# Performance work log

Measured on AMD Instinct MI355X. Metric: run time of the kernel, lower is better.

The kernel has to match this reference:

```python
import jax, jax.numpy as jnp
import numpy as np

B, S, DIM = 1, 1024, 1024
H, G = 16, 4
HPG = H // G
DK = 64
DV = 64
L_CMP, D_STR = 32, 16      # compression block length l, stride d
L_SEL, N_SEL = 64, 8       # selection block length, num selected blocks
W_WIN = 512                # sliding window
TAU = 1.0
GATE_H = 32
SCALE = 1.0 / float(np.sqrt(DK))
S_CMP = (S - L_CMP) // D_STR + 1          # number of compressed blocks
N_BLK = (S + L_SEL - 1) // L_SEL          # number of selection blocks

# static Eq.9 mapping: fractional overlap of compressed block c with selection block m
_c0 = np.arange(S_CMP) * D_STR
_m0 = np.arange(N_BLK) * L_SEL
_ov = np.maximum(0, np.minimum(_c0[:, None] + L_CMP, _m0[None, :] + L_SEL)
                 - np.maximum(_c0[:, None], _m0[None, :]))
M_MAP = jnp.asarray(_ov.astype(np.float32) / float(L_CMP))   # [S_CMP, N_BLK]

_POOL_IDX = np.arange(S_CMP)[:, None] * D_STR + np.arange(L_CMP)[None, :]  # [S_CMP, L_CMP]


def _rope(x, pos):
    # llama-style rotary embedding; pos broadcasts against x's leading dims
    half = x.shape[-1] // 2
    inv = 1.0 / (10000.0 ** (jnp.arange(half, dtype=jnp.float32) / half))
    ang = pos[..., None] * inv
    cos, sin = jnp.cos(ang), jnp.sin(ang)
    x1, x2 = x[..., :half], x[..., half:]
    return jnp.concatenate([x1 * cos - x2 * sin, x1 * sin + x2 * cos], axis=-1)


def _masked_softmax(scores, mask):
    p = jax.nn.softmax(jnp.where(mask, scores, -1e30), axis=-1)
    return jnp.where(mask.any(axis=-1, keepdims=True), p, 0.0)


def _forward(x, wq, wk_sel, wv_sel, wk_win, wv_win, wk_cmp, wv_cmp, w_out,
             g1_w, g1_b, g2_w, g2_b):
    pos = jnp.arange(S, dtype=jnp.float32)
    t = jnp.arange(S)
    q = _rope((x @ wq.T).reshape(B, S, G, HPG, DK), pos[None, :, None, None])  # [B,S,G,h,Dk]

    def k_proj(w):
        k = jnp.transpose((x @ w.T).reshape(B, S, G, DK), (0, 2, 1, 3))  # [B,G,S,Dk]
        return _rope(k, pos[None, None, :])

    def v_proj(w):
        return jnp.transpose((x @ w.T).reshape(B, S, G, DV), (0, 2, 1, 3))  # [B,G,S,Dv]

    # --- compressed branch (phi = avg pooling over blocks of l with stride d) ---
    k_cmp = k_proj(wk_cmp); v_cmp = v_proj(wv_cmp)
    Kc = k_cmp[:, :, _POOL_IDX, :].mean(axis=3)  # [B,G,S_CMP,Dk]
    Vc = v_cmp[:, :, _POOL_IDX, :].mean(axis=3)  # [B,G,S_CMP,Dv]
    sc_cmp = jnp.einsum('bsghd,bgcd->bsghc', q, Kc) * SCALE
    cmp_mask = (jnp.arange(S_CMP) * D_STR + (L_CMP - 1))[None, :] <= t[:, None]  # [S,S_CMP]
    p_cmp = _masked_softmax(sc_cmp, cmp_mask[None, :, None, None, :])
    O_cmp = jnp.einsum('bsghc,bgcd->bsghd', p_cmp, Vc)

    # --- selection branch: map compressed scores to selection blocks (Eq.9),
    #     group-sum over heads, force block 0 + current block, top-k, gather ---
    p_slc = jnp.einsum('bsghc,cm->bsgm', p_cmp, M_MAP)  # sums over heads h -> [B,S,G,N_BLK]
    blk = jnp.arange(N_BLK)
    forced = (blk[None, :] == 0) | (blk[None, :] == (t // L_SEL)[:, None])  # [S,N_BLK]
    causal = (blk[None, :] * L_SEL) <= t[:, None]                            # [S,N_BLK]
    sel_logits = jnp.where(causal[None, :, None, :],
                           p_slc + 1e6 * forced[None, :, None, :], -1e9)
    _, top_idx = jax.lax.top_k(sel_logits, N_SEL)  # [B,S,G,N_SEL]
    tok = (top_idx[..., None] * L_SEL + jnp.arange(L_SEL)).reshape(B, S, G, N_SEL * L_SEL)
    tok_g = jnp.transpose(tok, (0, 2, 1, 3))  # [B,G,S,L]
    k_sel = k_proj(wk_sel); v_sel = v_proj(wv_sel)
    bi = jnp.arange(B)[:, None, None, None]
    gi = jnp.arange(G)[None, :, None, None]
    Kg = k_sel[bi, gi, tok_g]  # [B,G,S,L,Dk]
    Vg = v_sel[bi, gi, tok_g]  # [B,G,S,L,Dv]
    sc_sel = jnp.einsum('bsghd,bgsld->bsghl', q, Kg) * SCALE
    tok_mask = (tok <= t[None, :, None, None])[:, :, :, None, :]  # causal within gathered tokens
    p_sel = _masked_softmax(sc_sel, tok_mask)
    O_sel = jnp.einsum('bsghl,bgsld->bsghd', p_sel, Vg)

    # --- sliding window branch ---
    k_win = k_proj(wk_win); v_win = v_proj(wv_win)
    sc_win = jnp.einsum('bsghd,bgtd->bsght', q, k_win) * SCALE
    wmask = (t[None, :] <= t[:, None]) & (t[None, :] > t[:, None] - W_WIN)  # [S,S]
    p_win = _masked_softmax(sc_win, wmask[None, :, None, None, :])
    O_win = jnp.einsum('bsght,bgtd->bsghd', p_win, v_win)

    # --- gate MLP on group-pooled q ---
    qg = q.mean(axis=3)                              # [B,S,G,Dk]
    h1 = jax.nn.silu(qg @ g1_w.T + g1_b)
    glog = (h1 @ g2_w.T + g2_b) / max(TAU, 1e-6)
    pg = jax.nn.softmax(glog, axis=-1)               # [B,S,G,3]
    top2 = jax.lax.top_k(glog, 2)[0]
    peaked = jax.lax.stop_gradient((top2[..., 0] - top2[..., 1]) > 50.0)
    onehot = jax.nn.one_hot(jnp.argmax(glog, axis=-1), 3, dtype=pg.dtype)
    pg = jnp.where(peaked[..., None], onehot, pg)

    O = (pg[..., 0][..., None, None] * O_cmp
         + pg[..., 1][..., None, None] * O_sel
         + pg[..., 2][..., None, None] * O_win)      # [B,S,G,h,Dv]
    return O.reshape(B, S, H * DV) @ w_out.T


def setup_inputs() -> dict:
    key = jax.random.key(0)
    ks = jax.random.split(key, 11)
    n = lambda k, shp, s=0.02: jax.random.normal(k, shp, dtype=jnp.float32) * s
    return {
        'x': jax.random.normal(ks[0], (B, S, DIM), dtype=jnp.float32),
        'wq': n(ks[1], (H * DK, DIM)),
        'wk_sel': n(ks[2], (G * DK, DIM)),
        'wv_sel': n(ks[3], (G * DV, DIM)),
        'wk_win': n(ks[4], (G * DK, DIM)),
        'wv_win': n(ks[5], (G * DV, DIM)),
        'wk_cmp': n(ks[6], (G * DK, DIM)),
        'wv_cmp': n(ks[7], (G * DV, DIM)),
        'w_out': n(ks[8], (DIM, H * DV)),
        'g1_w': n(ks[9], (GATE_H, DK), 0.1),
        'g1_b': jnp.zeros((GATE_H,), jnp.float32),
        'g2_w': n(ks[10], (3, GATE_H), 0.05),  # xavier gain 0.1 -> small init
        'g2_b': jnp.zeros((3,), jnp.float32),
    }


def reference(x, wq, wk_sel, wv_sel, wk_win, wv_win, wk_cmp, wv_cmp, w_out,
              g1_w, g1_b, g2_w, g2_b):
    return _forward(x, wq, wk_sel, wv_sel, wk_win, wv_win, wk_cmp, wv_cmp, w_out,
                    g1_w, g1_b, g2_w, g2_b)
```

## Files before the change

kernel.cpp:

```cpp
#include <hip/hip_runtime.h>
#include <math.h>

#define SLEN   1024
#define NGRP   4
#define NHEAD  16
#define HPGRP  4
#define DKV    64
#define SCMP   63
#define NBLK   16
#define NSELK  8
#define WWIN   512
#define SCALEF 0.125f
#define QBLK   16
#define EXPOFF 8.0f
#define CSTR   2560

typedef __attribute__((ext_vector_type(4))) float f32x4;
typedef __attribute__((ext_vector_type(8))) short bf16x8;

__device__ __forceinline__ unsigned short f2bf(float f) {
  unsigned u = __float_as_uint(f);
  u += 0x7FFFu + ((u >> 16) & 1u);
  return (unsigned short)(u >> 16);
}
__device__ __forceinline__ unsigned pack2(float a, float b) {
  return (unsigned)f2bf(a) | ((unsigned)f2bf(b) << 16);
}
__device__ __forceinline__ bf16x8 pack8(float4 a, float4 b) {
  union { bf16x8 v; unsigned u[4]; } u;
  u.u[0] = pack2(a.x, a.y); u.u[1] = pack2(a.z, a.w);
  u.u[2] = pack2(b.x, b.y); u.u[3] = pack2(b.z, b.w);
  return u.v;
}

struct ConvJobs {
  const float* src[9];
  unsigned* dst[9];
  int n4[9];
  int cnt;
};

__global__ __launch_bounds__(256) void conv_f32_bf16(ConvJobs jb) {
  const int stride = gridDim.x * blockDim.x;
  for (int t = 0; t < jb.cnt; ++t) {
    const float4* s = (const float4*)jb.src[t];
    uint2* d = (uint2*)jb.dst[t];
    const int n4 = jb.n4[t];
    for (int i = blockIdx.x * blockDim.x + threadIdx.x; i < n4; i += stride) {
      const float4 v = s[i];
      uint2 o;
      o.x = pack2(v.x, v.y);
      o.y = pack2(v.z, v.w);
      d[i] = o;
    }
  }
}

__global__ __launch_bounds__(256) void conv_add_bf16(
    const float* __restrict__ a, const float* __restrict__ b, uint2* __restrict__ d)
{
  const int i = blockIdx.x * 256 + threadIdx.x;
  const float4 va = ((const float4*)a)[i];
  const float4 vb = ((const float4*)b)[i];
  uint2 o;
  o.x = pack2(va.x + vb.x, va.y + vb.y);
  o.y = pack2(va.z + vb.z, va.w + vb.w);
  d[i] = o;
}

__device__ __forceinline__ void gload_lds16(const unsigned short* g, unsigned short* l) {
  __builtin_amdgcn_global_load_lds(
      (const __attribute__((address_space(1))) void*)g,
      (__attribute__((address_space(3))) void*)l, 16, 0, 0);
}

__device__ __forceinline__ void gemm_mfma_body(
    const unsigned short* __restrict__ A, const unsigned short* __restrict__ W,
    float* __restrict__ C, int N, int K, int bm, int bn, int tid)
{
  __shared__ unsigned short As[3][2048];
  __shared__ unsigned short Bs[3][2048];
  const int lane = tid & 63;
  const int wave = tid >> 6;
  const int wr = wave >> 1, wc = wave & 1;

  const int sub = tid >> 6;
  const int kh  = (tid >> 4) & 3;
  const int row = tid & 15;
  const unsigned short* aSrc = A + (size_t)(bm + sub * 16 + row) * K + kh * 8;
  const unsigned short* bSrc = W + (size_t)(bn + sub * 16 + row) * K + kh * 8;
  const int slot = tid * 8;

  f32x4 acc[2][2];
#pragma unroll
  for (int m = 0; m < 2; ++m)
#pragma unroll
    for (int n = 0; n < 2; ++n) acc[m][n] = (f32x4){0.f, 0.f, 0.f, 0.f};

  const int NIT = K >> 5;
  gload_lds16(aSrc + 0,  &As[0][slot]);
  gload_lds16(bSrc + 0,  &Bs[0][slot]);
  gload_lds16(aSrc + 32, &As[1][slot]);
  gload_lds16(bSrc + 32, &Bs[1][slot]);

  for (int i = 0; i < NIT; ++i) {
    __builtin_amdgcn_sched_barrier(0);
    if (i + 1 < NIT) asm volatile("s_waitcnt vmcnt(2)" ::: "memory");
    else             asm volatile("s_waitcnt vmcnt(0)" ::: "memory");
    __builtin_amdgcn_s_barrier();
    __builtin_amdgcn_sched_barrier(0);
    if (i + 2 < NIT) {
      const int nb = (i + 2) % 3;
      gload_lds16(aSrc + (i + 2) * 32, &As[nb][slot]);
      gload_lds16(bSrc + (i + 2) * 32, &Bs[nb][slot]);
    }
    const int cur = i % 3;
    const bf16x8 a0 = *(const bf16x8*)(&As[cur][(wr * 2 + 0) * 512 + lane * 8]);
    const bf16x8 a1 = *(const bf16x8*)(&As[cur][(wr * 2 + 1) * 512 + lane * 8]);
    const bf16x8 b0 = *(const bf16x8*)(&Bs[cur][(wc * 2 + 0) * 512 + lane * 8]);
    const bf16x8 b1 = *(const bf16x8*)(&Bs[cur][(wc * 2 + 1) * 512 + lane * 8]);
    acc[0][0] = __builtin_amdgcn_mfma_f32_16x16x32_bf16(a0, b0, acc[0][0], 0, 0, 0);
    acc[0][1] = __builtin_amdgcn_mfma_f32_16x16x32_bf16(a0, b1, acc[0][1], 0, 0, 0);
    acc[1][0] = __builtin_amdgcn_mfma_f32_16x16x32_bf16(a1, b0, acc[1][0], 0, 0, 0);
    acc[1][1] = __builtin_amdgcn_mfma_f32_16x16x32_bf16(a1, b1, acc[1][1], 0, 0, 0);
  }

  const int cr = (lane >> 4) * 4;
  const int cc = lane & 15;
#pragma unroll
  for (int m = 0; m < 2; ++m)
#pragma unroll
    for (int n = 0; n < 2; ++n) {
      float* cp = C + (size_t)(bm + wr * 32 + m * 16 + cr) * N + (bn + wc * 32 + n * 16 + cc);
#pragma unroll
      for (int r = 0; r < 4; ++r) cp[(size_t)r * N] = acc[m][n][r];
    }
}

__global__ __launch_bounds__(256) void gemm_bf16(
    const unsigned short* __restrict__ A, const unsigned short* __restrict__ W,
    float* __restrict__ C, int N, int K)
{
  gemm_mfma_body(A, W, C, N, K, blockIdx.y * 64, blockIdx.x * 64, threadIdx.x);
}

__global__ __launch_bounds__(256) void mid_kernel(
    const float* __restrict__ C,
    const float* __restrict__ g1w, const float* __restrict__ g1b,
    const float* __restrict__ g2w, const float* __restrict__ g2b,
    unsigned short* __restrict__ q_b,
    unsigned short* __restrict__ kselb, unsigned short* __restrict__ kwinb,
    float* __restrict__ gates,
    unsigned short* __restrict__ vselT, unsigned short* __restrict__ vwinT,
    unsigned short* __restrict__ KcB, unsigned short* __restrict__ VcTB)
{
  const int b = blockIdx.x;
  const int t = threadIdx.x;

  __shared__ float csS[32], snS[32];
  __shared__ float qs[1024];
  __shared__ float qgS[4][64];
  __shared__ float h1S[4][32];
  __shared__ float glS[4][3];
  __shared__ float tile[32][33];
  __shared__ float csP[32][32], snP[32][32];

  if (b < 1024) {
    const int s = b;
    if (t < 32) {
      const float inv = powf(10000.f, -(float)t * (1.f / 32.f));
      float sn, cs;
      sincosf((float)s * inv, &sn, &cs);
      csS[t] = cs; snS[t] = sn;
    }
    __syncthreads();
    {
      const int ht = t >> 4;
      const float* qr = C + (size_t)s * CSTR + ht * 64;
#pragma unroll
      for (int i = 0; i < 2; ++i) {
        const int dd = (t & 15) * 2 + i;
        const float x1 = qr[dd], x2 = qr[dd + 32];
        qs[ht * 64 + dd]      = x1 * csS[dd] - x2 * snS[dd];
        qs[ht * 64 + dd + 32] = x1 * snS[dd] + x2 * csS[dd];
      }
    }
    {
      const int which = t >> 7;
      const int g = (t >> 5) & 3, dd = t & 31;
      const float* src = C + (size_t)s * CSTR + (which ? 1536 : 1024) + g * 64;
      unsigned short* dst = (which ? kwinb : kselb) + (size_t)s * 256 + g * 64;
      const float x1 = src[dd], x2 = src[dd + 32];
      dst[dd]      = f2bf(x1 * csS[dd] - x2 * snS[dd]);
      dst[dd + 32] = f2bf(x1 * snS[dd] + x2 * csS[dd]);
    }
    __syncthreads();
    {
      uint2 o;
      o.x = pack2(qs[t * 4 + 0], qs[t * 4 + 1]);
      o.y = pack2(qs[t * 4 + 2], qs[t * 4 + 3]);
      *(uint2*)(q_b + (size_t)s * 1024 + t * 4) = o;
    }
    {
      const int g = t >> 6, d = t & 63;
      qgS[g][d] = (qs[g * 256 + d] + qs[g * 256 + 64 + d] +
                   qs[g * 256 + 128 + d] + qs[g * 256 + 192 + d]) * 0.25f;
    }
    __syncthreads();
    if (t < 128) {
      const int g = t >> 5, j = t & 31;
      float a = g1b[j];
      for (int d = 0; d < 64; ++d) a += qgS[g][d] * g1w[j * 64 + d];
      h1S[g][j] = a / (1.f + expf(-a));
    }
    __syncthreads();
    if (t < 16) {
      const int g = t >> 2, rr = t & 3;
      if (rr < 3) {
        float a = g2b[rr];
        for (int j = 0; j < 32; ++j) a += h1S[g][j] * g2w[rr * 32 + j];
        glS[g][rr] = a;
      }
    }
    __syncthreads();
    if (t < 4) {
      const int g = t;
      const float gl0 = glS[g][0], gl1 = glS[g][1], gl2 = glS[g][2];
      const float m1 = fmaxf(gl0, fmaxf(gl1, gl2));
      const float e0 = expf(gl0 - m1), e1 = expf(gl1 - m1), e2 = expf(gl2 - m1);
      const float inv = 1.f / (e0 + e1 + e2);
      float p0 = e0 * inv, p1 = e1 * inv, p2 = e2 * inv;
      int am = 0; float best = gl0;
      if (gl1 > best) { best = gl1; am = 1; }
      if (gl2 > best) { best = gl2; am = 2; }
      float second = -INFINITY;
      if (am != 0) second = fmaxf(second, gl0);
      if (am != 1) second = fmaxf(second, gl1);
      if (am != 2) second = fmaxf(second, gl2);
      if (best - second > 50.f) {
        p0 = (am == 0) ? 1.f : 0.f; p1 = (am == 1) ? 1.f : 0.f; p2 = (am == 2) ? 1.f : 0.f;
      }
      float* o = gates + (size_t)(s * 4 + g) * 3;
      o[0] = p0; o[1] = p1; o[2] = p2;
    }
  } else if (b < 1536) {
    const int idx = b - 1024;
    const int tr = (idx & 31) * 32, tc = ((idx >> 5) & 7) * 32;
    const int z = idx >> 8;
    const int off = z ? 1792 : 1280;
    unsigned short* dst = z ? vwinT : vselT;
    const int r = t >> 5, c = t & 31;
#pragma unroll
    for (int i = 0; i < 4; ++i)
      tile[r + i * 8][c] = C[(size_t)(tr + r + i * 8) * CSTR + off + tc + c];
    __syncthreads();
#pragma unroll
    for (int i = 0; i < 4; ++i)
      dst[(size_t)(tc + r + i * 8) * 1024 + tr + c] = f2bf(tile[c][r + i * 8]);
  } else {
    const int c = b - 1536;
    const int g = t >> 6, d = t & 63;
#pragma unroll
    for (int qq = 0; qq < 4; ++qq) {
      const int idx = t * 4 + qq;
      const int j = idx >> 5, dd = idx & 31;
      const float inv = powf(10000.f, -(float)dd * (1.f / 32.f));
      float sn, cs;
      sincosf((float)(c * 16 + j) * inv, &sn, &cs);
      csP[j][dd] = cs; snP[j][dd] = sn;
    }
    __syncthreads();
    float ak = 0.f, av = 0.f;
    if (c < SCMP) {
      const int d2 = d & 31;
      for (int j = 0; j < 32; ++j) {
        const int pos = c * 16 + j;
        const float k1 = C[(size_t)pos * CSTR + 2048 + g * 64 + d2];
        const float k2 = C[(size_t)pos * CSTR + 2048 + g * 64 + d2 + 32];
        ak += (d < 32) ? (k1 * csP[j][d2] - k2 * snP[j][d2])
                       : (k1 * snP[j][d2] + k2 * csP[j][d2]);
        av += C[(size_t)pos * CSTR + 2304 + g * 64 + d];
      }
      ak *= (1.f / 32.f); av *= (1.f / 32.f);
    }
    KcB[(size_t)(g * 64 + c) * 64 + d] = f2bf(ak);
    VcTB[(size_t)(g * 64 + d) * 64 + c] = f2bf(av);
  }
}

__device__ __forceinline__ void stage_tile(
    const unsigned short* kbase, int krow,
    const unsigned short* vbase, int vrow,
    unsigned short* Kb, unsigned short* Vb, int tid)
{
#pragma unroll
  for (int i = 0; i < 2; ++i) {
    const int t2 = tid + i * 256;
    const int sf = t2 >> 7, sks = (t2 >> 6) & 1, skh = (t2 >> 4) & 3, stk = t2 & 15;
    gload_lds16(kbase + (size_t)(16 * sf + stk) * krow + sks * 32 + skh * 8, Kb + t2 * 8);
    gload_lds16(vbase + (size_t)(16 * sf + stk) * vrow + sks * 32 + skh * 8, Vb + t2 * 8);
  }
}

template<int BR>
__device__ __forceinline__ void attn_compute(
    int b, int s0, int l,
    bf16x8 aq0, bf16x8 aq1,
    float (&ps)[4], f32x4 (&Oa)[4],
    const unsigned short* Klds, const unsigned short* Vlds,
    float (*Pw)[68], const unsigned* selmaskS)
{
  const int kg = l >> 4, lr = l & 15;
  f32x4 sc[4];
  __builtin_amdgcn_s_setprio(1);
#pragma unroll
  for (int f = 0; f < 4; ++f) {
    sc[f] = (f32x4){0.f, 0.f, 0.f, 0.f};
    sc[f] = __builtin_amdgcn_mfma_f32_16x16x32_bf16(
        aq0, *(const bf16x8*)(Klds + (f * 2 + 0) * 512 + l * 8), sc[f], 0, 0, 0);
    sc[f] = __builtin_amdgcn_mfma_f32_16x16x32_bf16(
        aq1, *(const bf16x8*)(Klds + (f * 2 + 1) * 512 + l * 8), sc[f], 0, 0, 0);
  }
  __builtin_amdgcn_s_setprio(0);

#pragma unroll
  for (int r = 0; r < 4; ++r) {
    const int lrow = kg * 4 + r;
    const int sr = s0 + lrow;
#pragma unroll
    for (int f = 0; f < 4; ++f) {
      const int tok = b * 64 + 16 * f + lr;
      bool ok;
      if (BR == 0)      ok = (tok < SCMP) && (tok * 16 + 31 <= sr);
      else if (BR == 1) ok = ((selmaskS[lrow] >> b) & 1u) && (tok <= sr);
      else              ok = (tok <= sr) && (tok > sr - WWIN);
      const float p = ok ? __expf(sc[f][r] * SCALEF - EXPOFF) : 0.f;
      Pw[lrow][16 * f + lr] = p;
      ps[r] += p;
    }
  }
  asm volatile("s_waitcnt lgkmcnt(0)" ::: "memory");
#pragma unroll
  for (int ks = 0; ks < 2; ++ks) {
    const float4 pa0 = *(const float4*)&Pw[lr][ks * 32 + kg * 8];
    const float4 pa1 = *(const float4*)&Pw[lr][ks * 32 + kg * 8 + 4];
    const bf16x8 pa = pack8(pa0, pa1);
    __builtin_amdgcn_s_setprio(1);
#pragma unroll
    for (int f = 0; f < 4; ++f)
      Oa[f] = __builtin_amdgcn_mfma_f32_16x16x32_bf16(
          pa, *(const bf16x8*)(Vlds + (f * 2 + ks) * 512 + l * 8), Oa[f], 0, 0, 0);
    __builtin_amdgcn_s_setprio(0);
  }
}

#define TILE_SYNC(more) do { \
    __builtin_amdgcn_sched_barrier(0); \
    if (more) asm volatile("s_waitcnt vmcnt(4)" ::: "memory"); \
    else      asm volatile("s_waitcnt vmcnt(0)" ::: "memory"); \
    __builtin_amdgcn_sched_barrier(0); \
    __builtin_amdgcn_s_barrier(); \
    __builtin_amdgcn_sched_barrier(0); \
  } while (0)

__global__ __launch_bounds__(256) void attn_mfma_kernel(
    const unsigned short* __restrict__ qb,
    const unsigned short* __restrict__ kselb,
    const unsigned short* __restrict__ vselT,
    const unsigned short* __restrict__ kwinb,
    const unsigned short* __restrict__ vwinT,
    const unsigned short* __restrict__ KcB,
    const unsigned short* __restrict__ VcTB,
    const float* __restrict__ gates,
    float* __restrict__ Ocs, float* __restrict__ Owin)
{
  const int qt = blockIdx.x;
  const int g  = blockIdx.y;
  const int z  = blockIdx.z;
  const int s0 = qt * QBLK;
  const int tid = threadIdx.x;
  const int w = tid >> 6, l = tid & 63;
  const int kg = l >> 4, lr = l & 15;
  const int bmax = s0 >> 6;

  __shared__ unsigned short Klds[3][4096];
  __shared__ unsigned short Vlds[3][4096];
  __shared__ float Plds[4][16][68];
  __shared__ float lgS[QBLK][16];
  __shared__ float lcS[4][16];
  __shared__ unsigned selmaskS[QBLK];
  __shared__ int selListS[16];
  __shared__ int nselS;

  if (tid < QBLK) selmaskS[tid] = 0u;

  const int sq = s0 + lr;
  const unsigned short* qrow = qb + (size_t)(sq * 16 + g * 4 + w) * 64;
  const bf16x8 aq0 = *(const bf16x8*)(qrow + kg * 8);
  const bf16x8 aq1 = *(const bf16x8*)(qrow + 32 + kg * 8);

  float gv[3][4];
#pragma unroll
  for (int r = 0; r < 4; ++r) {
    const int sr = s0 + kg * 4 + r;
    const float* gp = gates + (size_t)(sr * 4 + g) * 3;
    gv[0][r] = gp[0]; gv[1][r] = gp[1]; gv[2][r] = gp[2];
  }

  f32x4 Ot[4];
#pragma unroll
  for (int f = 0; f < 4; ++f) Ot[f] = (f32x4){0.f, 0.f, 0.f, 0.f};

  float ps[4], ls[4];
  f32x4 Oa[4];

#define ARESET() do { \
    _Pragma("unroll") for (int r = 0; r < 4; ++r) ps[r] = 0.f; \
    _Pragma("unroll") for (int f = 0; f < 4; ++f) Oa[f] = (f32x4){0.f,0.f,0.f,0.f}; \
  } while (0)
#define REDUCE_LS() do { \
    _Pragma("unroll") for (int r = 0; r < 4; ++r) { \
      ls[r] = ps[r]; \
      ls[r] += __shfl_xor(ls[r], 1); ls[r] += __shfl_xor(ls[r], 2); \
      ls[r] += __shfl_xor(ls[r], 4); ls[r] += __shfl_xor(ls[r], 8); } \
  } while (0)
#define AFINAL(bi) do { \
    _Pragma("unroll") for (int f = 0; f < 4; ++f) \
    _Pragma("unroll") for (int r = 0; r < 4; ++r) \
      Ot[f][r] += gv[bi][r] * ((ls[r] > 0.f) ? (Oa[f][r] / ls[r]) : 0.f); \
  } while (0)

  if (z == 0) {
    ARESET();
    stage_tile(KcB + (size_t)g * 64 * 64, 64, VcTB + (size_t)g * 64 * 64, 64,
               Klds[0], Vlds[0], tid);
    TILE_SYNC(0);
    attn_compute<0>(0, s0, l, aq0, aq1, ps, Oa, Klds[0], Vlds[0], Plds[w], selmaskS);
    REDUCE_LS();
    if ((l & 15) == 0) {
#pragma unroll
      for (int r = 0; r < 4; ++r) lcS[w][kg * 4 + r] = ls[r];
    }
    AFINAL(0);
    __syncthreads();

    {
      const int row = tid >> 4, mm = tid & 15;
      float psl = 0.f;
#pragma unroll
      for (int hh = 0; hh < 4; ++hh) {
        const float lc = lcS[hh][row];
        if (lc > 0.f) {
          const int cb = 4 * mm;
          float a = Plds[hh][row][cb] + Plds[hh][row][cb + 1] + Plds[hh][row][cb + 2];
          if (cb >= 1)       a += 0.5f * Plds[hh][row][cb - 1];
          if (cb + 3 < SCMP) a += 0.5f * Plds[hh][row][cb + 3];
          psl += a / lc;
        }
      }
      const bool causal = (mm <= bmax);
      const bool forced = (mm == 0) || (mm == bmax);
      lgS[row][mm] = causal ? (psl + (forced ? 1e6f : 0.f)) : -1e9f;
    }
    __syncthreads();
    {
      const int row = tid >> 4, mm = tid & 15;
      const float my = lgS[row][mm];
      int rank = 0;
#pragma unroll
      for (int m2 = 0; m2 < 16; ++m2) {
        const float v = lgS[row][m2];
        if (v > my || (v == my && m2 < mm)) ++rank;
      }
      if (rank < NSELK && mm <= bmax) atomicOr(&selmaskS[row], 1u << mm);
    }
    __syncthreads();
    if (tid == 0) {
      unsigned u = 0;
      for (int r = 0; r < QBLK; ++r) u |= selmaskS[r];
      int n = 0;
      for (int b = 0; b < 16; ++b) if ((u >> b) & 1u) selListS[n++] = b;
      nselS = n;
    }
    __syncthreads();
    const int nt = nselS;

    ARESET();
    {
      const int b0 = selListS[0];
      stage_tile(kselb + (size_t)b0 * 64 * 256 + g * 64, 256,
                 vselT + (size_t)g * 64 * 1024 + b0 * 64, 1024,
                 Klds[0], Vlds[0], tid);
      for (int i = 0; i < nt; ++i) {
        if (i + 1 < nt) {
          const int bn = selListS[i + 1];
          const int nb = (i + 1) % 3;
          stage_tile(kselb + (size_t)bn * 64 * 256 + g * 64, 256,
                     vselT + (size_t)g * 64 * 1024 + bn * 64, 1024,
                     Klds[nb], Vlds[nb], tid);
        }
        TILE_SYNC(i + 1 < nt);
        attn_compute<1>(selListS[i], s0, l, aq0, aq1, ps, Oa,
                        Klds[i % 3], Vlds[i % 3], Plds[w], selmaskS);
        __builtin_amdgcn_sched_barrier(0);
      }
    }
    REDUCE_LS();
    AFINAL(1);

#pragma unroll
    for (int f = 0; f < 4; ++f)
#pragma unroll
      for (int r = 0; r < 4; ++r) {
        const int sr = s0 + kg * 4 + r;
        Ocs[(size_t)(sr * 16 + g * 4 + w) * 64 + 16 * f + lr] = Ot[f][r];
      }
  } else {
    ARESET();
    const int blo = (s0 >= (WWIN - 1)) ? ((s0 - (WWIN - 1)) >> 6) : 0;
    const int nt = bmax - blo + 1;
    stage_tile(kwinb + (size_t)blo * 64 * 256 + g * 64, 256,
               vwinT + (size_t)g * 64 * 1024 + blo * 64, 1024,
               Klds[0], Vlds[0], tid);
    for (int i = 0; i < nt; ++i) {
      if (i + 1 < nt) {
        const int bn = blo + i + 1;
        const int nb = (i + 1) % 3;
        stage_tile(kwinb + (size_t)bn * 64 * 256 + g * 64, 256,
                   vwinT + (size_t)g * 64 * 1024 + bn * 64, 1024,
                   Klds[nb], Vlds[nb], tid);
      }
      TILE_SYNC(i + 1 < nt);
      attn_compute<2>(blo + i, s0, l, aq0, aq1, ps, Oa,
                      Klds[i % 3], Vlds[i % 3], Plds[w], selmaskS);
      __builtin_amdgcn_sched_barrier(0);
    }
    REDUCE_LS();
    AFINAL(2);

#pragma unroll
    for (int f = 0; f < 4; ++f)
#pragma unroll
      for (int r = 0; r < 4; ++r) {
        const int sr = s0 + kg * 4 + r;
        Owin[(size_t)(sr * 16 + g * 4 + w) * 64 + 16 * f + lr] = Ot[f][r];
      }
  }
#undef ARESET
#undef REDUCE_LS
#undef AFINAL
}

extern "C" void kernel_launch(void* const* d_in, const int* in_sizes, int n_in,
                              void* d_out, int out_size, void* d_ws, size_t ws_size,
                              hipStream_t stream) {
  const float* x      = (const float*)d_in[0];
  const float* wq     = (const float*)d_in[1];
  const float* wk_sel = (const float*)d_in[2];
  const float* wv_sel = (const float*)d_in[3];
  const float* wk_win = (const float*)d_in[4];
  const float* wv_win = (const float*)d_in[5];
  const float* wk_cmp = (const float*)d_in[6];
  const float* wv_cmp = (const float*)d_in[7];
  const float* w_out  = (const float*)d_in[8];
  const float* g1w    = (const float*)d_in[9];
  const float* g1b    = (const float*)d_in[10];
  const float* g2w    = (const float*)d_in[11];
  const float* g2b    = (const float*)d_in[12];

  float* ws = (float*)d_ws;
  float* Cq    = ws;
  float* gts   = Cq + 2621440;
  float* Ocs   = gts + 12288;
  float* Owin  = Ocs + 1048576;

  unsigned short* xb     = (unsigned short*)(Owin + 1048576);
  unsigned short* wqkvb  = xb + 1048576;
  unsigned short* w_outb = wqkvb + 2621440;
  unsigned short* q_b    = w_outb + 1048576;
  unsigned short* kselb  = q_b + 1048576;
  unsigned short* kwinb  = kselb + 262144;
  unsigned short* vselT  = kwinb + 262144;
  unsigned short* vwinT  = vselT + 262144;
  unsigned short* KcB    = vwinT + 262144;
  unsigned short* VcTB   = KcB + 16384;

  ConvJobs j1 = {};
  j1.cnt = 9;
  j1.src[0] = x;      j1.dst[0] = (unsigned*)xb;                        j1.n4[0] = 262144;
  j1.src[1] = wq;     j1.dst[1] = (unsigned*)wqkvb;                     j1.n4[1] = 262144;
  j1.src[2] = wk_sel; j1.dst[2] = (unsigned*)(wqkvb + 1048576);         j1.n4[2] = 65536;
  j1.src[3] = wv_sel; j1.dst[3] = (unsigned*)(wqkvb + 1048576+262144);  j1.n4[3] = 65536;
  j1.src[4] = wk_win; j1.dst[4] = (unsigned*)(wqkvb + 1048576+524288);  j1.n4[4] = 65536;
  j1.src[5] = wv_win; j1.dst[5] = (unsigned*)(wqkvb + 1048576+786432);  j1.n4[5] = 65536;
  j1.src[6] = wk_cmp; j1.dst[6] = (unsigned*)(wqkvb + 1048576+1048576); j1.n4[6] = 65536;
  j1.src[7] = wv_cmp; j1.dst[7] = (unsigned*)(wqkvb + 1048576+1310720); j1.n4[7] = 65536;
  j1.src[8] = w_out;  j1.dst[8] = (unsigned*)w_outb;                    j1.n4[8] = 262144;
  conv_f32_bf16<<<1024, 256, 0, stream>>>(j1);

  gemm_bf16<<<dim3(40, 16), 256, 0, stream>>>(xb, wqkvb, Cq, CSTR, 1024);

  mid_kernel<<<1600, 256, 0, stream>>>(Cq, g1w, g1b, g2w, g2b,
                                       q_b, kselb, kwinb, gts,
                                       vselT, vwinT, KcB, VcTB);

  attn_mfma_kernel<<<dim3(64, 4, 2), 256, 0, stream>>>(
      q_b, kselb, vselT, kwinb, vwinT, KcB, VcTB, gts, Ocs, Owin);

  conv_add_bf16<<<1024, 256, 0, stream>>>(Ocs, Owin, (uint2*)xb);
  gemm_bf16<<<dim3(16, 16), 256, 0, stream>>>(xb, w_outb, (float*)d_out, 1024, 1024);
}
```

Before: 112.7 us.

## Split attention into compressed pass and split-K selected/window tile kernel with combine

The fused attention kernel is split into three kernels. The first computes the compressed branch and top-k block selection and writes the selection masks to global memory. The second processes selected and window tiles with work split in two per branch, giving four z-slices instead of two, and writes unnormalised numerators and row sums. A combine kernel then normalises, gates, sums and converts the result to bf16. Probabilities are also stored to LDS as bf16 rather than fp32. The aim is to balance load across blocks and raise parallelism, at the cost of an extra launch and roughly 16 MB of partial-result traffic.

After: 115.1 us. 2.1% more time.

```diff
diff --git a/kernel.cpp b/kernel.cpp
--- a/kernel.cpp
+++ b/kernel.cpp
@@ -54,18 +54,6 @@
       d[i] = o;
     }
   }
-}
-
-__global__ __launch_bounds__(256) void conv_add_bf16(
-    const float* __restrict__ a, const float* __restrict__ b, uint2* __restrict__ d)
-{
-  const int i = blockIdx.x * 256 + threadIdx.x;
-  const float4 va = ((const float4*)a)[i];
-  const float4 vb = ((const float4*)b)[i];
-  uint2 o;
-  o.x = pack2(va.x + vb.x, va.y + vb.y);
-  o.y = pack2(va.z + vb.z, va.w + vb.w);
-  d[i] = o;
 }
 
 __device__ __forceinline__ void gload_lds16(const unsigned short* g, unsigned short* l) {
@@ -302,58 +290,6 @@
   }
 }
 
-template<int BR>
-__device__ __forceinline__ void attn_compute(
-    int b, int s0, int l,
-    bf16x8 aq0, bf16x8 aq1,
-    float (&ps)[4], f32x4 (&Oa)[4],
-    const unsigned short* Klds, const unsigned short* Vlds,
-    float (*Pw)[68], const unsigned* selmaskS)
-{
-  const int kg = l >> 4, lr = l & 15;
-  f32x4 sc[4];
-  __builtin_amdgcn_s_setprio(1);
-#pragma unroll
-  for (int f = 0; f < 4; ++f) {
-    sc[f] = (f32x4){0.f, 0.f, 0.f, 0.f};
-    sc[f] = __builtin_amdgcn_mfma_f32_16x16x32_bf16(
-        aq0, *(const bf16x8*)(Klds + (f * 2 + 0) * 512 + l * 8), sc[f], 0, 0, 0);
-    sc[f] = __builtin_amdgcn_mfma_f32_16x16x32_bf16(
-        aq1, *(const bf16x8*)(Klds + (f * 2 + 1) * 512 + l * 8), sc[f], 0, 0, 0);
-  }
-  __builtin_amdgcn_s_setprio(0);
-
-#pragma unroll
-  for (int r = 0; r < 4; ++r) {
-    const int lrow = kg * 4 + r;
-    const int sr = s0 + lrow;
-#pragma unroll
-    for (int f = 0; f < 4; ++f) {
-      const int tok = b * 64 + 16 * f + lr;
-      bool ok;
-      if (BR == 0)      ok = (tok < SCMP) && (tok * 16 + 31 <= sr);
-      else if (BR == 1) ok = ((selmaskS[lrow] >> b) & 1u) && (tok <= sr);
-      else              ok = (tok <= sr) && (tok > sr - WWIN);
-      const float p = ok ? __expf(sc[f][r] * SCALEF - EXPOFF) : 0.f;
-      Pw[lrow][16 * f + lr] = p;
-      ps[r] += p;
-    }
-  }
-  asm volatile("s_waitcnt lgkmcnt(0)" ::: "memory");
-#pragma unroll
-  for (int ks = 0; ks < 2; ++ks) {
-    const float4 pa0 = *(const float4*)&Pw[lr][ks * 32 + kg * 8];
-    const float4 pa1 = *(const float4*)&Pw[lr][ks * 32 + kg * 8 + 4];
-    const bf16x8 pa = pack8(pa0, pa1);
-    __builtin_amdgcn_s_setprio(1);
-#pragma unroll
-    for (int f = 0; f < 4; ++f)
-      Oa[f] = __builtin_amdgcn_mfma_f32_16x16x32_bf16(
-          pa, *(const bf16x8*)(Vlds + (f * 2 + ks) * 512 + l * 8), Oa[f], 0, 0, 0);
-    __builtin_amdgcn_s_setprio(0);
-  }
-}
-
 #define TILE_SYNC(more) do { \
     __builtin_amdgcn_sched_barrier(0); \
     if (more) asm volatile("s_waitcnt vmcnt(4)" ::: "memory"); \
@@ -363,16 +299,199 @@
     __builtin_amdgcn_sched_barrier(0); \
   } while (0)
 
-__global__ __launch_bounds__(256) void attn_mfma_kernel(
+__global__ __launch_bounds__(256) void attn_cmp_kernel(
+    const unsigned short* __restrict__ qb,
+    const unsigned short* __restrict__ KcB,
+    const unsigned short* __restrict__ VcTB,
+    const float* __restrict__ gates,
+    float* __restrict__ Ocs, unsigned* __restrict__ selmaskG)
+{
+  const int qt = blockIdx.x;
+  const int g  = blockIdx.y;
+  const int s0 = qt * QBLK;
+  const int tid = threadIdx.x;
+  const int w = tid >> 6, l = tid & 63;
+  const int kg = l >> 4, lr = l & 15;
+  const int bmax = s0 >> 6;
+
+  __shared__ unsigned short Klds[4096];
+  __shared__ unsigned short Vlds[4096];
+  __shared__ float Plds[4][16][68];
+  __shared__ float lgS[QBLK][16];
+  __shared__ float lcS[4][16];
+  __shared__ unsigned selmaskS[QBLK];
+
+  if (tid < QBLK) selmaskS[tid] = 0u;
+
+  const int sq = s0 + lr;
+  const unsigned short* qrow = qb + (size_t)(sq * 16 + g * 4 + w) * 64;
+  const bf16x8 aq0 = *(const bf16x8*)(qrow + kg * 8);
+  const bf16x8 aq1 = *(const bf16x8*)(qrow + 32 + kg * 8);
+
+  float gv0[4];
+#pragma unroll
+  for (int r = 0; r < 4; ++r)
+    gv0[r] = gates[(size_t)((s0 + kg * 4 + r) * 4 + g) * 3];
+
+  float ps[4], ls[4];
+  f32x4 Oa[4];
+#pragma unroll
+  for (int r = 0; r < 4; ++r) ps[r] = 0.f;
+#pragma unroll
+  for (int f = 0; f < 4; ++f) Oa[f] = (f32x4){0.f, 0.f, 0.f, 0.f};
+
+  stage_tile(KcB + (size_t)g * 64 * 64, 64, VcTB + (size_t)g * 64 * 64, 64,
+             Klds, Vlds, tid);
+  TILE_SYNC(0);
+
+  f32x4 sc[4];
+  __builtin_amdgcn_s_setprio(1);
+#pragma unroll
+  for (int f = 0; f < 4; ++f) {
+    sc[f] = (f32x4){0.f, 0.f, 0.f, 0.f};
+    sc[f] = __builtin_amdgcn_mfma_f32_16x16x32_bf16(
+        aq0, *(const bf16x8*)(Klds + (f * 2 + 0) * 512 + l * 8), sc[f], 0, 0, 0);
+    sc[f] = __builtin_amdgcn_mfma_f32_16x16x32_bf16(
+        aq1, *(const bf16x8*)(Klds + (f * 2 + 1) * 512 + l * 8), sc[f], 0, 0, 0);
+  }
+  __builtin_amdgcn_s_setprio(0);
+#pragma unroll
+  for (int r = 0; r < 4; ++r) {
+    const int sr = s0 + kg * 4 + r;
+#pragma unroll
+    for (int f = 0; f < 4; ++f) {
+      const int tok = 16 * f + lr;
+      const bool ok = (tok < SCMP) && (tok * 16 + 31 <= sr);
+      const float p = ok ? __expf(sc[f][r] * SCALEF - EXPOFF) : 0.f;
+      Plds[w][kg * 4 + r][16 * f + lr] = p;
+      ps[r] += p;
+    }
+  }
+  asm volatile("s_waitcnt lgkmcnt(0)" ::: "memory");
+#pragma unroll
+  for (int ks = 0; ks < 2; ++ks) {
+    const float4 pa0 = *(const float4*)&Plds[w][lr][ks * 32 + kg * 8];
+    const float4 pa1 = *(const float4*)&Plds[w][lr][ks * 32 + kg * 8 + 4];
+    const bf16x8 pa = pack8(pa0, pa1);
+    __builtin_amdgcn_s_setprio(1);
+#pragma unroll
+    for (int f = 0; f < 4; ++f)
+      Oa[f] = __builtin_amdgcn_mfma_f32_16x16x32_bf16(
+          pa, *(const bf16x8*)(Vlds + (f * 2 + ks) * 512 + l * 8), Oa[f], 0, 0, 0);
+    __builtin_amdgcn_s_setprio(0);
+  }
+
+#pragma unroll
+  for (int r = 0; r < 4; ++r) {
+    ls[r] = ps[r];
+    ls[r] += __shfl_xor(ls[r], 1); ls[r] += __shfl_xor(ls[r], 2);
+    ls[r] += __shfl_xor(ls[r], 4); ls[r] += __shfl_xor(ls[r], 8);
+  }
+  if ((l & 15) == 0) {
+#pragma unroll
+    for (int r = 0; r < 4; ++r) lcS[w][kg * 4 + r] = ls[r];
+  }
+#pragma unroll
+  for (int f = 0; f < 4; ++f)
+#pragma unroll
+    for (int r = 0; r < 4; ++r) {
+      const int sr = s0 + kg * 4 + r;
+      Ocs[(size_t)(sr * 16 + g * 4 + w) * 64 + 16 * f + lr] =
+          gv0[r] * ((ls[r] > 0.f) ? (Oa[f][r] / ls[r]) : 0.f);
+    }
+  __syncthreads();
+
+  {
+    const int row = tid >> 4, mm = tid & 15;
+    float psl = 0.f;
+#pragma unroll
+    for (int hh = 0; hh < 4; ++hh) {
+      const float lc = lcS[hh][row];
+      if (lc > 0.f) {
+        const int cb = 4 * mm;
+        float a = Plds[hh][row][cb] + Plds[hh][row][cb + 1] + Plds[hh][row][cb + 2];
+        if (cb >= 1)       a += 0.5f * Plds[hh][row][cb - 1];
+        if (cb + 3 < SCMP) a += 0.5f * Plds[hh][row][cb + 3];
+        psl += a / lc;
+      }
+    }
+    const bool causal = (mm <= bmax);
+    const bool forced = (mm == 0) || (mm == bmax);
+    lgS[row][mm] = causal ? (psl + (forced ? 1e6f : 0.f)) : -1e9f;
+  }
+  __syncthreads();
+  {
+    const int row = tid >> 4, mm = tid & 15;
+    const float my = lgS[row][mm];
+    int rank = 0;
+#pragma unroll
+    for (int m2 = 0; m2 < 16; ++m2) {
+      const float v = lgS[row][m2];
+      if (v > my || (v == my && m2 < mm)) ++rank;
+    }
+    if (rank < NSELK && mm <= bmax) atomicOr(&selmaskS[row], 1u << mm);
+  }
+  __syncthreads();
+  if (tid < QBLK) selmaskG[(s0 + tid) * 4 + g] = selmaskS[tid];
+}
+
+template<int BR>
+__device__ __forceinline__ void attn_computeB(
+    int b, int s0, int l,
+    bf16x8 aq0, bf16x8 aq1,
+    float (&ps)[4], f32x4 (&Oa)[4],
+    const unsigned short* Klds, const unsigned short* Vlds,
+    unsigned short (*PwB)[72], const unsigned* selmaskS)
+{
+  const int kg = l >> 4, lr = l & 15;
+  f32x4 sc[4];
+  __builtin_amdgcn_s_setprio(1);
+#pragma unroll
+  for (int f = 0; f < 4; ++f) {
+    sc[f] = (f32x4){0.f, 0.f, 0.f, 0.f};
+    sc[f] = __builtin_amdgcn_mfma_f32_16x16x32_bf16(
+        aq0, *(const bf16x8*)(Klds + (f * 2 + 0) * 512 + l * 8), sc[f], 0, 0, 0);
+    sc[f] = __builtin_amdgcn_mfma_f32_16x16x32_bf16(
+        aq1, *(const bf16x8*)(Klds + (f * 2 + 1) * 512 + l * 8), sc[f], 0, 0, 0);
+  }
+  __builtin_amdgcn_s_setprio(0);
+
+#pragma unroll
+  for (int r = 0; r < 4; ++r) {
+    const int lrow = kg * 4 + r;
+    const int sr = s0 + lrow;
+#pragma unroll
+    for (int f = 0; f < 4; ++f) {
+      const int tok = b * 64 + 16 * f + lr;
+      bool ok;
+      if (BR == 1) ok = ((selmaskS[lrow] >> b) & 1u) && (tok <= sr);
+      else         ok = (tok <= sr) && (tok > sr - WWIN);
+      const float p = ok ? __expf(sc[f][r] * SCALEF - EXPOFF) : 0.f;
+      PwB[lrow][16 * f + lr] = f2bf(p);
+      ps[r] += p;
+    }
+  }
+  asm volatile("s_waitcnt lgkmcnt(0)" ::: "memory");
+#pragma unroll
+  for (int ks = 0; ks < 2; ++ks) {
+    const bf16x8 pa = *(const bf16x8*)&PwB[lr][ks * 32 + kg * 8];
+    __builtin_amdgcn_s_setprio(1);
+#pragma unroll
+    for (int f = 0; f < 4; ++f)
+      Oa[f] = __builtin_amdgcn_mfma_f32_16x16x32_bf16(
+          pa, *(const bf16x8*)(Vlds + (f * 2 + ks) * 512 + l * 8), Oa[f], 0, 0, 0);
+    __builtin_amdgcn_s_setprio(0);
+  }
+}
+
+__global__ __launch_bounds__(256) void attn_tiles_kernel(
     const unsigned short* __restrict__ qb,
     const unsigned short* __restrict__ kselb,
     const unsigned short* __restrict__ vselT,
     const unsigned short* __restrict__ kwinb,
     const unsigned short* __restrict__ vwinT,
-    const unsigned short* __restrict__ KcB,
-    const unsigned short* __restrict__ VcTB,
-    const float* __restrict__ gates,
-    float* __restrict__ Ocs, float* __restrict__ Owin)
+    const unsigned* __restrict__ selmaskG,
+    float* __restrict__ Pnum, float* __restrict__ Pls)
 {
   const int qt = blockIdx.x;
   const int g  = blockIdx.y;
@@ -382,173 +501,130 @@
   const int w = tid >> 6, l = tid & 63;
   const int kg = l >> 4, lr = l & 15;
   const int bmax = s0 >> 6;
+  const bool isSel = (z < 2);
 
   __shared__ unsigned short Klds[3][4096];
   __shared__ unsigned short Vlds[3][4096];
-  __shared__ float Plds[4][16][68];
-  __shared__ float lgS[QBLK][16];
-  __shared__ float lcS[4][16];
+  __shared__ unsigned short PldsB[4][16][72];
   __shared__ unsigned selmaskS[QBLK];
-  __shared__ int selListS[16];
-  __shared__ int nselS;
-
-  if (tid < QBLK) selmaskS[tid] = 0u;
+  __shared__ int listS[16];
+  __shared__ int ntS;
+
+  if (tid < QBLK)
+    selmaskS[tid] = isSel ? selmaskG[(s0 + tid) * 4 + g] : 0u;
+  __syncthreads();
+  if (tid == 0) {
+    int n = 0;
+    if (isSel) {
+      unsigned u = 0;
+      for (int r = 0; r < QBLK; ++r) u |= selmaskS[r];
+      int idx = 0;
+      for (int b = 0; b < 16; ++b)
+        if ((u >> b) & 1u) { if ((idx & 1) == z) listS[n++] = b; ++idx; }
+    } else {
+      const int blo = (s0 >= (WWIN - 1)) ? ((s0 - (WWIN - 1)) >> 6) : 0;
+      for (int b = blo + (z - 2); b <= bmax; b += 2) listS[n++] = b;
+    }
+    ntS = n;
+  }
+  __syncthreads();
+  const int nt = ntS;
 
   const int sq = s0 + lr;
   const unsigned short* qrow = qb + (size_t)(sq * 16 + g * 4 + w) * 64;
   const bf16x8 aq0 = *(const bf16x8*)(qrow + kg * 8);
   const bf16x8 aq1 = *(const bf16x8*)(qrow + 32 + kg * 8);
 
-  float gv[3][4];
-#pragma unroll
-  for (int r = 0; r < 4; ++r) {
-    const int sr = s0 + kg * 4 + r;
-    const float* gp = gates + (size_t)(sr * 4 + g) * 3;
-    gv[0][r] = gp[0]; gv[1][r] = gp[1]; gv[2][r] = gp[2];
-  }
-
-  f32x4 Ot[4];
-#pragma unroll
-  for (int f = 0; f < 4; ++f) Ot[f] = (f32x4){0.f, 0.f, 0.f, 0.f};
+  const unsigned short* kb = isSel ? kselb : kwinb;
+  const unsigned short* vb = isSel ? vselT : vwinT;
 
   float ps[4], ls[4];
   f32x4 Oa[4];
-
-#define ARESET() do { \
-    _Pragma("unroll") for (int r = 0; r < 4; ++r) ps[r] = 0.f; \
-    _Pragma("unroll") for (int f = 0; f < 4; ++f) Oa[f] = (f32x4){0.f,0.f,0.f,0.f}; \
-  } while (0)
-#define REDUCE_LS() do { \
-    _Pragma("unroll") for (int r = 0; r < 4; ++r) { \
-      ls[r] = ps[r]; \
-      ls[r] += __shfl_xor(ls[r], 1); ls[r] += __shfl_xor(ls[r], 2); \
-      ls[r] += __shfl_xor(ls[r], 4); ls[r] += __shfl_xor(ls[r], 8); } \
-  } while (0)
-#define AFINAL(bi) do { \
-    _Pragma("unroll") for (int f = 0; f < 4; ++f) \
-    _Pragma("unroll") for (int r = 0; r < 4; ++r) \
-      Ot[f][r] += gv[bi][r] * ((ls[r] > 0.f) ? (Oa[f][r] / ls[r]) : 0.f); \
-  } while (0)
-
-  if (z == 0) {
-    ARESET();
-    stage_tile(KcB + (size_t)g * 64 * 64, 64, VcTB + (size_t)g * 64 * 64, 64,
-               Klds[0], Vlds[0], tid);
-    TILE_SYNC(0);
-    attn_compute<0>(0, s0, l, aq0, aq1, ps, Oa, Klds[0], Vlds[0], Plds[w], selmaskS);
-    REDUCE_LS();
-    if ((l & 15) == 0) {
-#pragma unroll
-      for (int r = 0; r < 4; ++r) lcS[w][kg * 4 + r] = ls[r];
-    }
-    AFINAL(0);
-    __syncthreads();
-
-    {
-      const int row = tid >> 4, mm = tid & 15;
-      float psl = 0.f;
-#pragma unroll
-      for (int hh = 0; hh < 4; ++hh) {
-        const float lc = lcS[hh][row];
-        if (lc > 0.f) {
-          const int cb = 4 * mm;
-          float a = Plds[hh][row][cb] + Plds[hh][row][cb + 1] + Plds[hh][row][cb + 2];
-          if (cb >= 1)       a += 0.5f * Plds[hh][row][cb - 1];
-          if (cb + 3 < SCMP) a += 0.5f * Plds[hh][row][cb + 3];
-          psl += a / lc;
-        }
-      }
-      const bool causal = (mm <= bmax);
-      const bool forced = (mm == 0) || (mm == bmax);
-      lgS[row][mm] = causal ? (psl + (forced ? 1e6f : 0.f)) : -1e9f;
-    }
-    __syncthreads();
-    {
-      const int row = tid >> 4, mm = tid & 15;
-      const float my = lgS[row][mm];
-      int rank = 0;
-#pragma unroll
-      for (int m2 = 0; m2 < 16; ++m2) {
-        const float v = lgS[row][m2];
-        if (v > my || (v == my && m2 < mm)) ++rank;
-      }
-      if (rank < NSELK && mm <= bmax) atomicOr(&selmaskS[row], 1u << mm);
-    }
-    __syncthreads();
-    if (tid == 0) {
-      unsigned u = 0;
-      for (int r = 0; r < QBLK; ++r) u |= selmaskS[r];
-      int n = 0;
-      for (int b = 0; b < 16; ++b) if ((u >> b) & 1u) selListS[n++] = b;
-      nselS = n;
-    }
-    __syncthreads();
-    const int nt = nselS;
-
-    ARESET();
-    {
-      const int b0 = selListS[0];
-      stage_tile(kselb + (size_t)b0 * 64 * 256 + g * 64, 256,
-                 vselT + (size_t)g * 64 * 1024 + b0 * 64, 1024,
-                 Klds[0], Vlds[0], tid);
-      for (int i = 0; i < nt; ++i) {
-        if (i + 1 < nt) {
-          const int bn = selListS[i + 1];
-          const int nb = (i + 1) % 3;
-          stage_tile(kselb + (size_t)bn * 64 * 256 + g * 64, 256,
-                     vselT + (size_t)g * 64 * 1024 + bn * 64, 1024,
-                     Klds[nb], Vlds[nb], tid);
-        }
-        TILE_SYNC(i + 1 < nt);
-        attn_compute<1>(selListS[i], s0, l, aq0, aq1, ps, Oa,
-                        Klds[i % 3], Vlds[i % 3], Plds[w], selmaskS);
-        __builtin_amdgcn_sched_barrier(0);
-      }
-    }
-    REDUCE_LS();
-    AFINAL(1);
-
-#pragma unroll
-    for (int f = 0; f < 4; ++f)
-#pragma unroll
-      for (int r = 0; r < 4; ++r) {
-        const int sr = s0 + kg * 4 + r;
-        Ocs[(size_t)(sr * 16 + g * 4 + w) * 64 + 16 * f + lr] = Ot[f][r];
-      }
-  } else {
-    ARESET();
-    const int blo = (s0 >= (WWIN - 1)) ? ((s0 - (WWIN - 1)) >> 6) : 0;
-    const int nt = bmax - blo + 1;
-    stage_tile(kwinb + (size_t)blo * 64 * 256 + g * 64, 256,
-               vwinT + (size_t)g * 64 * 1024 + blo * 64, 1024,
+#pragma unroll
+  for (int r = 0; r < 4; ++r) ps[r] = 0.f;
+#pragma unroll
+  for (int f = 0; f < 4; ++f) Oa[f] = (f32x4){0.f, 0.f, 0.f, 0.f};
+
+  if (nt > 0) {
+    const int b0 = listS[0];
+    stage_tile(kb + (size_t)b0 * 64 * 256 + g * 64, 256,
+               vb + (size_t)g * 64 * 1024 + b0 * 64, 1024,
                Klds[0], Vlds[0], tid);
     for (int i = 0; i < nt; ++i) {
       if (i + 1 < nt) {
-        const int bn = blo + i + 1;
+        const int bn = listS[i + 1];
         const int nb = (i + 1) % 3;
-        stage_tile(kwinb + (size_t)bn * 64 * 256 + g * 64, 256,
-                   vwinT + (size_t)g * 64 * 1024 + bn * 64, 1024,
+        stage_tile(kb + (size_t)bn * 64 * 256 + g * 64, 256,
+                   vb + (size_t)g * 64 * 1024 + bn * 64, 1024,
                    Klds[nb], Vlds[nb], tid);
       }
       TILE_SYNC(i + 1 < nt);
-      attn_compute<2>(blo + i, s0, l, aq0, aq1, ps, Oa,
-                      Klds[i % 3], Vlds[i % 3], Plds[w], selmaskS);
+      if (isSel)
+        attn_computeB<1>(listS[i], s0, l, aq0, aq1, ps, Oa,
+                         Klds[i % 3], Vlds[i % 3], PldsB[w], selmaskS);
+      else
+        attn_computeB<2>(listS[i], s0, l, aq0, aq1, ps, Oa,
+                         Klds[i % 3], Vlds[i % 3], PldsB[w], selmaskS);
       __builtin_amdgcn_sched_barrier(0);
     }
-    REDUCE_LS();
-    AFINAL(2);
-
-#pragma unroll
-    for (int f = 0; f < 4; ++f)
-#pragma unroll
-      for (int r = 0; r < 4; ++r) {
-        const int sr = s0 + kg * 4 + r;
-        Owin[(size_t)(sr * 16 + g * 4 + w) * 64 + 16 * f + lr] = Ot[f][r];
-      }
-  }
-#undef ARESET
-#undef REDUCE_LS
-#undef AFINAL
+  }
+
+#pragma unroll
+  for (int r = 0; r < 4; ++r) {
+    ls[r] = ps[r];
+    ls[r] += __shfl_xor(ls[r], 1); ls[r] += __shfl_xor(ls[r], 2);
+    ls[r] += __shfl_xor(ls[r], 4); ls[r] += __shfl_xor(ls[r], 8);
+  }
+
+  float* np = Pnum + (size_t)z * 1048576;
+#pragma unroll
+  for (int f = 0; f < 4; ++f)
+#pragma unroll
+    for (int r = 0; r < 4; ++r) {
+      const int sr = s0 + kg * 4 + r;
+      np[(size_t)(sr * 16 + g * 4 + w) * 64 + 16 * f + lr] = Oa[f][r];
+    }
+  if ((l & 15) == 0) {
+#pragma unroll
+    for (int r = 0; r < 4; ++r)
+      Pls[(size_t)z * 16384 + (s0 + kg * 4 + r) * 16 + g * 4 + w] = ls[r];
+  }
+}
+
+__global__ __launch_bounds__(256) void combine_kernel(
+    const float* __restrict__ Ocs,
+    const float* __restrict__ Pnum, const float* __restrict__ Pls,
+    const float* __restrict__ gates, uint2* __restrict__ xb)
+{
+  const int s = blockIdx.x;
+  const int t = threadIdx.x;
+  const int hg = t >> 4, d4 = (t & 15) * 4;
+  const int g = hg >> 2;
+  const size_t base = (size_t)(s * 16 + hg) * 64 + d4;
+
+  const float4 oc = *(const float4*)(Ocs + base);
+  const float4 n0 = *(const float4*)(Pnum + 0 * 1048576 + base);
+  const float4 n1 = *(const float4*)(Pnum + 1 * 1048576 + base);
+  const float4 n2 = *(const float4*)(Pnum + 2 * 1048576 + base);
+  const float4 n3 = *(const float4*)(Pnum + 3 * 1048576 + base);
+
+  const int li = s * 16 + hg;
+  const float lsel = Pls[0 * 16384 + li] + Pls[1 * 16384 + li];
+  const float lwin = Pls[2 * 16384 + li] + Pls[3 * 16384 + li];
+  const float* gp = gates + (size_t)(s * 4 + g) * 3;
+  const float c1 = (lsel > 0.f) ? (gp[1] / lsel) : 0.f;
+  const float c2 = (lwin > 0.f) ? (gp[2] / lwin) : 0.f;
+
+  float4 o;
+  o.x = oc.x + c1 * (n0.x + n1.x) + c2 * (n2.x + n3.x);
+  o.y = oc.y + c1 * (n0.y + n1.y) + c2 * (n2.y + n3.y);
+  o.z = oc.z + c1 * (n0.z + n1.z) + c2 * (n2.z + n3.z);
+  o.w = oc.w + c1 * (n0.w + n1.w) + c2 * (n2.w + n3.w);
+
+  uint2 r;
+  r.x = pack2(o.x, o.y);
+  r.y = pack2(o.z, o.w);
+  xb[base >> 2] = r;
 }
 
 extern "C" void kernel_launch(void* const* d_in, const int* in_sizes, int n_in,
@@ -572,9 +648,11 @@
   float* Cq    = ws;
   float* gts   = Cq + 2621440;
   float* Ocs   = gts + 12288;
-  float* Owin  = Ocs + 1048576;
-
-  unsigned short* xb     = (unsigned short*)(Owin + 1048576);
+  float* Pnum  = Ocs + 1048576;
+  float* Pls   = Pnum + 4194304;
+  unsigned* selG = (unsigned*)(Pls + 65536);
+
+  unsigned short* xb     = (unsigned short*)(selG + 4096);
   unsigned short* wqkvb  = xb + 1048576;
   unsigned short* w_outb = wqkvb + 2621440;
   unsigned short* q_b    = w_outb + 1048576;
@@ -604,9 +682,12 @@
                                        q_b, kselb, kwinb, gts,
                                        vselT, vwinT, KcB, VcTB);
 
-  attn_mfma_kernel<<<dim3(64, 4, 2), 256, 0, stream>>>(
-      q_b, kselb, vselT, kwinb, vwinT, KcB, VcTB, gts, Ocs, Owin);
-
-  conv_add_bf16<<<1024, 256, 0, stream>>>(Ocs, Owin, (uint2*)xb);
+  attn_cmp_kernel<<<dim3(64, 4), 256, 0, stream>>>(q_b, KcB, VcTB, gts, Ocs, selG);
+
+  attn_tiles_kernel<<<dim3(64, 4, 4), 256, 0, stream>>>(
+      q_b, kselb, vselT, kwinb, vwinT, selG, Pnum, Pls);
+
+  combine_kernel<<<1024, 256, 0, stream>>>(Ocs, Pnum, Pls, gts, (uint2*)xb);
+
   gemm_bf16<<<dim3(16, 16), 256, 0, stream>>>(xb, w_outb, (float*)d_out, 1024, 1024);
 }
```
